# Optimization experiments

Hardware: AMD Instinct MI355X
Metric: run time of the kernel (lower is better)

## Reference

```python
import jax, jax.numpy as jnp
import numpy as np

B, S, D, H, F, E, K = 2, 2048, 1024, 16, 4096, 8, 2
EPS = 1e-6


def setup_inputs() -> dict:
    key = jax.random.key(0)
    ks = jax.random.split(key, 9)
    s = 0.02
    return {
        "x": jax.random.normal(ks[0], (B, S, D), jnp.float32),
        "n1_w": jnp.ones((D,), jnp.float32),
        "n2_w": jnp.ones((D,), jnp.float32),
        "wq": jax.random.normal(ks[1], (D, D), jnp.float32) * s,
        "wk": jax.random.normal(ks[2], (D, D), jnp.float32) * s,
        "wv": jax.random.normal(ks[3], (D, D), jnp.float32) * s,
        "wo": jax.random.normal(ks[4], (D, D), jnp.float32) * s,
        "router_w": jax.random.normal(ks[5], (E, D), jnp.float32) * s,  # nn.Linear(D, E, bias=False)
        "w1": jax.random.normal(ks[6], (E, D, F), jnp.float32) * s,
        "b1": jnp.zeros((E, F), jnp.float32),
        "w2": jax.random.normal(ks[7], (E, F, D), jnp.float32) * s,
        "b2": jnp.zeros((E, D), jnp.float32),
    }


def _rms(t, w):
    return t * w * jax.lax.rsqrt(jnp.mean(t * t, axis=-1, keepdims=True) + EPS)


def reference(x, n1_w, n2_w, wq, wk, wv, wo, router_w, w1, b1, w2, b2):
    hd = D // H
    # --- pre-norm causal multi-head self-attention ---
    h = _rms(x, n1_w)
    q = (h @ wq).reshape(B, S, H, hd)
    k = (h @ wk).reshape(B, S, H, hd)
    v = (h @ wv).reshape(B, S, H, hd)
    scores = jnp.einsum("bqhd,bkhd->bhqk", q, k) * (hd ** -0.5)
    causal = jnp.tril(jnp.ones((S, S), bool))
    scores = jnp.where(causal, scores, jnp.float32(-1e9))
    attn = jax.nn.softmax(scores, axis=-1)
    attn_out = jnp.einsum("bhqk,bkhd->bqhd", attn, v).reshape(B, S, D) @ wo
    x = x + attn_out
    # --- pre-norm MoE MLP: dense experts + top-k weighted combine ---
    h2 = _rms(x, n2_w)
    logits = h2 @ router_w.T                         # [B,S,E]
    probs = jax.nn.softmax(logits, axis=-1)
    topv, topi = jax.lax.top_k(probs, K)             # [B,S,K]
    topv = topv / jnp.sum(topv, axis=-1, keepdims=True)  # renormalized top-k gates
    bi = jnp.arange(B)[:, None, None]
    si = jnp.arange(S)[None, :, None]
    gates = jnp.zeros_like(probs).at[bi, si, topi].set(topv)  # sparse gates [B,S,E]
    eh = jax.nn.gelu(jnp.einsum("bsd,edf->ebsf", h2, w1) + b1[:, None, None, :])
    eo = jnp.einsum("ebsf,efd->ebsd", eh, w2) + b2[:, None, None, :]
    y = jnp.einsum("ebsd,bse->bsd", eo, gates)
    return x + y
```

## Files before the change

kernel.cpp:

```cpp
#include <hip/hip_runtime.h>
#include <hip/hip_bf16.h>


typedef float fx4 __attribute__((ext_vector_type(4)));
typedef short sx4 __attribute__((ext_vector_type(4)));
typedef short sx8 __attribute__((ext_vector_type(8)));
typedef int ix2 __attribute__((ext_vector_type(2)));
typedef int ix4 __attribute__((ext_vector_type(4)));

#define DEVFN static __device__ __forceinline__
#define MFMA16(a, b, c) __builtin_amdgcn_mfma_f32_16x16x32_bf16((a), (b), (c), 0, 0, 0)

typedef __attribute__((address_space(1))) const void GASV;
typedef __attribute__((address_space(3))) void LASV;

DEVFN short f2bf(float f) {
  unsigned u = __float_as_uint(f);
  return (short)((u + 0x7FFFu + ((u >> 16) & 1u)) >> 16);
}
DEVFN float bf2f(short s) { return __uint_as_float(((unsigned)(unsigned short)s) << 16); }

DEVFN int cvt_pk_bf16(float a, float b) {
  int r;
  asm("v_cvt_pk_bf16_f32 %0, %1, %2" : "=v"(r) : "v"(a), "v"(b));
  return r;
}

DEVFN void gll16(const short* g, short* l) {
  __builtin_amdgcn_global_load_lds((GASV*)g, (LASV*)l, 16, 0, 0);
}

template <int BK>
DEVFN int swzr(int row) {
  if constexpr (BK == 64)
    return row & 7;
  else
    return (row ^ (row >> 2)) & 3;
}

DEVFN float fast_gelu(float x) {
  float u = 0.7978845608028654f * (x + 0.044715f * x * x * x);
  float e = __expf(2.0f * u);
  float t = 1.0f - 2.0f / (1.0f + e);
  return 0.5f * x * (1.0f + t);
}

DEVFN float wsum64(float v) {
#pragma unroll
  for (int m = 1; m < 64; m <<= 1) v += __shfl_xor(v, m);
  return v;
}

template <int SPLIT>
__global__ __launch_bounds__(256) void transpose_k(const float* in, short* oh, short* ol,
                                                   int R, int C) {
  __shared__ float t[64][65];
  const int c0 = blockIdx.x * 64, r0 = blockIdx.y * 64;
  const long long bofs = (long long)blockIdx.z * R * C;
  in += bofs;
  oh += bofs;
  if (SPLIT) ol += bofs;
  const int tid = threadIdx.x;
  const int rr = tid >> 4, cc4 = (tid & 15) * 4;
#pragma unroll
  for (int i = 0; i < 4; ++i) {
    int r = i * 16 + rr;
    fx4 v = *(const fx4*)(in + (long long)(r0 + r) * C + c0 + cc4);
    t[r][cc4] = v.x;
    t[r][cc4 + 1] = v.y;
    t[r][cc4 + 2] = v.z;
    t[r][cc4 + 3] = v.w;
  }
  __syncthreads();
#pragma unroll
  for (int i = 0; i < 4; ++i) {
    int oc = i * 16 + rr;
    sx4 hv, lv;
#pragma unroll
    for (int j = 0; j < 4; ++j) {
      float v = t[cc4 + j][oc];
      short hi = f2bf(v);
      hv[j] = hi;
      if (SPLIT) lv[j] = f2bf(v - bf2f(hi));
    }
    *(sx4*)(oh + (long long)(c0 + oc) * R + r0 + cc4) = hv;
    if (SPLIT) *(sx4*)(ol + (long long)(c0 + oc) * R + r0 + cc4) = lv;
  }
}

template <int SPLIT>
__global__ __launch_bounds__(256) void rms_k(const float* x, const float* w, short* hh,
                                             short* hl) {
  const int row = blockIdx.x, tid = threadIdx.x;
  const fx4 v = ((const fx4*)(x + (long long)row * 1024))[tid];
  float ss = v.x * v.x + v.y * v.y + v.z * v.z + v.w * v.w;
  ss = wsum64(ss);
  __shared__ float red[4];
  if ((tid & 63) == 0) red[tid >> 6] = ss;
  __syncthreads();
  ss = red[0] + red[1] + red[2] + red[3];
  const float rr = rsqrtf(ss * (1.0f / 1024.0f) + 1e-6f);
  const fx4 wv = ((const fx4*)w)[tid];
  float vals[4] = {v.x * wv.x * rr, v.y * wv.y * rr, v.z * wv.z * rr, v.w * wv.w * rr};
  sx4 oh, ol;
#pragma unroll
  for (int c = 0; c < 4; ++c) {
    short hi = f2bf(vals[c]);
    oh[c] = hi;
    if (SPLIT) ol[c] = f2bf(vals[c] - bf2f(hi));
  }
  ((sx4*)(hh + (long long)row * 1024))[tid] = oh;
  if (SPLIT) ((sx4*)(hl + (long long)row * 1024))[tid] = ol;
}

struct GemmArgs {
  const short *Ah, *Al, *Bh, *Bl;
  int K, lda, ldb, ldc;
  long long strideBe;
  short *out_h, *out_l;
  float* out_f;
  const float* bias;
  const int* tile_info;
  const float* row_gate;
  const int* row_token;
};

template <int TERMS, int BM, int BK, int BN, int EPI, int PIPE>
__global__ __launch_bounds__(256) void gemm_k(GemmArgs a) {
  const int tid = threadIdx.x, lane = tid & 63, wave = tid >> 6;
  const int gx = gridDim.x;
  const int nwg = gx * (int)gridDim.y;
  int flat = (int)blockIdx.y * gx + (int)blockIdx.x;
  flat = (flat & 7) * (nwg >> 3) + (flat >> 3);
  const int bx = flat % gx;
  const int by = flat / gx;

  int row0, expert = 0, valid = BM;
  if constexpr (EPI == 3 || EPI == 5) {
    const int* ti = a.tile_info + by * 4;
    expert = ti[0];
    row0 = ti[1];
    valid = ti[2];
    if (valid == 0) return;
  } else {
    row0 = by * BM;
  }
  const short* Ap = a.Ah;
  const short* Bp = a.Bh + ((EPI == 3 || EPI == 5) ? (long long)expert * a.strideBe : 0ll);
  const int kbeg = blockIdx.z * a.K;

  constexpr int CH = BK / 8;
  constexpr int NIA = (BM * CH) / 256;
  constexpr int NIB = (BN * CH) / 256;
  constexpr int ASZ = BM * BK;
  constexpr int BSZ = BN * BK;
  constexpr int MI = BM / 32;
  constexpr int TN = BN / 32;
  constexpr int NB = PIPE ? 2 : 1;

  __shared__ short Ash[NB][ASZ];
  __shared__ short Bsh[NB][BSZ];
  __shared__ short Asl[TERMS == 3 ? NB : 1][TERMS == 3 ? ASZ : 1];
  __shared__ short Bsl[TERMS == 3 ? NB : 1][TERMS == 3 ? BSZ : 1];

  fx4 acc[MI][TN] = {};
  const int wr = wave >> 1, wc = wave & 1;

  long long aoff[NIA];
#pragma unroll
  for (int i = 0; i < NIA; ++i) {
    int row = (i * 256 + tid) / CH;
    if constexpr (EPI == 3)
      aoff[i] = (long long)a.row_token[row0 + row] * a.lda;
    else
      aoff[i] = (long long)(row0 + row) * a.lda;
  }

  auto stage = [&](int s, int k0) {
#pragma unroll
    for (int i = 0; i < NIA; ++i) {
      int t = i * 256 + tid;
      int row = t / CH, c = t % CH;
      int cc = c ^ swzr<BK>(row);
      int lbase = (i * 256 + wave * 64) * 8;
      long long acol = kbeg + k0 + cc * 8;
      gll16(Ap + aoff[i] + acol, &Ash[s][lbase]);
      if constexpr (TERMS == 3)
        gll16(a.Al + aoff[i] + acol, &Asl[s][lbase]);
    }
#pragma unroll
    for (int i = 0; i < NIB; ++i) {
      int t = i * 256 + tid;
      int row = t / CH, c = t % CH;
      int cc = c ^ swzr<BK>(row);
      int lbase = (i * 256 + wave * 64) * 8;
      long long acol = kbeg + k0 + cc * 8;
      gll16(Bp + (long long)(bx * BN + row) * a.ldb + acol, &Bsh[s][lbase]);
      if constexpr (TERMS == 3)
        gll16(a.Bl + (long long)(bx * BN + row) * a.ldb + acol, &Bsl[s][lbase]);
    }
  };

  auto compute = [&](int s) {
#pragma unroll
    for (int kk = 0; kk < BK / 32; ++kk) {
      sx8 ah[MI], bh[TN], al_[MI], bl_[TN];
#pragma unroll
      for (int mi = 0; mi < MI; ++mi) {
        int row = wr * (BM / 2) + mi * 16 + (lane & 15);
        int sc = (kk * 4 + (lane >> 4)) ^ swzr<BK>(row);
        ah[mi] = *(const sx8*)&Ash[s][row * BK + sc * 8];
        if constexpr (TERMS == 3) al_[mi] = *(const sx8*)&Asl[s][row * BK + sc * 8];
      }
#pragma unroll
      for (int ni = 0; ni < TN; ++ni) {
        int row = wc * (BN / 2) + ni * 16 + (lane & 15);
        int sc = (kk * 4 + (lane >> 4)) ^ swzr<BK>(row);
        bh[ni] = *(const sx8*)&Bsh[s][row * BK + sc * 8];
        if constexpr (TERMS == 3) bl_[ni] = *(const sx8*)&Bsl[s][row * BK + sc * 8];
      }
#pragma unroll
      for (int mi = 0; mi < MI; ++mi)
#pragma unroll
        for (int ni = 0; ni < TN; ++ni) {
          acc[mi][ni] = MFMA16(ah[mi], bh[ni], acc[mi][ni]);
          if constexpr (TERMS == 3) {
            acc[mi][ni] = MFMA16(ah[mi], bl_[ni], acc[mi][ni]);
            acc[mi][ni] = MFMA16(al_[mi], bh[ni], acc[mi][ni]);
          }
        }
    }
  };

  const int NT = a.K / BK;
  stage(0, 0);
  __syncthreads();
  for (int t = 0; t < NT; ++t) {
    if constexpr (PIPE) {
      if (t + 1 < NT) stage((t + 1) & 1, (t + 1) * BK);
      compute(t & 1);
      if (t + 1 < NT) __syncthreads();
    } else {
      compute(0);
      if (t + 1 < NT) {
        __syncthreads();
        stage(0, (t + 1) * BK);
        __syncthreads();
      }
    }
  }

#pragma unroll
  for (int mi = 0; mi < MI; ++mi)
#pragma unroll
    for (int ni = 0; ni < TN; ++ni) {
      fx4 v = acc[mi][ni];
      int rl = wr * (BM / 2) + mi * 16 + ((lane >> 4) << 2);
      int col = bx * BN + wc * (BN / 2) + ni * 16 + (lane & 15);
#pragma unroll
      for (int j = 0; j < 4; ++j) {
        int r = rl + j;
        long long grow = (long long)row0 + r;
        float xv = v[j];
        if constexpr (EPI == 1) {
          short hi = f2bf(xv);
          a.out_h[grow * a.ldc + col] = hi;
          a.out_l[grow * a.ldc + col] = f2bf(xv - bf2f(hi));
        } else if constexpr (EPI == 3) {
          xv += a.bias[expert * a.ldc + col];
          a.out_h[grow * a.ldc + col] = f2bf(fast_gelu(xv));
        } else if constexpr (EPI == 5) {
          if (r < valid) {
            xv += a.bias[expert * a.ldc + col];
            float g = a.row_gate[grow];
            a.out_h[grow * a.ldc + col] = f2bf(xv * g);
          }
        } else if constexpr (EPI == 6) {
          a.out_f[(long long)blockIdx.z * 4194304 + grow * a.ldc + col] = xv;
        }
      }
    }
}

__global__ __launch_bounds__(256) void combine_wo_k(const float* p0, const float* p1,
                                                    const float* resid, float* out) {
  const long long i = ((long long)blockIdx.x * 256 + threadIdx.x) * 4;
  fx4 a = *(const fx4*)(p0 + i);
  fx4 b = *(const fx4*)(p1 + i);
  fx4 r = *(const fx4*)(resid + i);
  fx4 o;
#pragma unroll
  for (int j = 0; j < 4; ++j) o[j] = a[j] + b[j] + r[j];
  *(fx4*)(out + i) = o;
}

__global__ __launch_bounds__(256) void combine_k(const int* row_of_entry,
                                                 const short* eo, float* out) {
  const int tid = threadIdx.x, lane = tid & 63, wave = tid >> 6;
  const long long token = (long long)blockIdx.x * 4 + wave;
  const int r1 = row_of_entry[token * 2];
  const int r2 = row_of_entry[token * 2 + 1];
  const sx8* e1 = (const sx8*)(eo + (long long)r1 * 1024);
  const sx8* e2 = (const sx8*)(eo + (long long)r2 * 1024);
  float* op = out + token * 1024;
#pragma unroll
  for (int half = 0; half < 2; ++half) {
    sx8 va = e1[lane + half * 64];
    sx8 vb = e2[lane + half * 64];
    int cb = (lane + half * 64) * 8;
#pragma unroll
    for (int q = 0; q < 2; ++q) {
      fx4 o = *(const fx4*)(op + cb + q * 4);
#pragma unroll
      for (int j = 0; j < 4; ++j) o[j] += bf2f(va[q * 4 + j]) + bf2f(vb[q * 4 + j]);
      *(fx4*)(op + cb + q * 4) = o;
    }
  }
}

__global__ __launch_bounds__(128, 2) void flash_k(const short* __restrict__ qkv_h,
                                                  const short* __restrict__ qkv_l,
                                                  short* __restrict__ ao_h,
                                                  short* __restrict__ ao_l) {
  const int tid = threadIdx.x, lane = tid & 63, wave = tid >> 6;
  const int l15 = lane & 15, g = lane >> 4;
  const int qt = (blockIdx.x + blockIdx.y) & 31;
  const int bh = blockIdx.y;
  const int b = bh >> 4, h = bh & 15;
  const long long base = (long long)b * 2048 * 3072;
  const int qw = qt * 64 + wave * 32;

  __shared__ short Kh[4096], Kl[4096];
  __shared__ int VTh[64 * 34], VTl[64 * 34];

  sx8 qh[2][2], ql[2][2];
#pragma unroll
  for (int mb = 0; mb < 2; ++mb)
#pragma unroll
    for (int kk = 0; kk < 2; ++kk) {
      long long qofs =
          base + (long long)(qw + mb * 16 + l15) * 3072 + h * 64 + kk * 32 + g * 8;
      qh[mb][kk] = *(const sx8*)(qkv_h + qofs);
      ql[mb][kk] = *(const sx8*)(qkv_l + qofs);
    }

  fx4 o[2][4] = {};
  float m_r[2] = {-3e38f, -3e38f}, l_r[2] = {0.f, 0.f};

  const int krow0 = tid >> 3;
  const int kc8 = (tid & 7) * 8;
  const int kswz = ((tid & 7) ^ (krow0 & 7)) * 8;
  const int vu = tid >> 3;
  const int vd0 = (tid & 7) * 8;

  sx8 kr[4], krl[4], vr[4], vrl[4];

  auto load_tile = [&](int kt2) {
    const long long tb = base + (long long)(kt2 * 64) * 3072 + h * 64;
#pragma unroll
    for (int s = 0; s < 4; ++s) {
      long long gofs = tb + 1024 + (long long)(s * 16 + krow0) * 3072 + kc8;
      kr[s] = *(const sx8*)(qkv_h + gofs);
      krl[s] = *(const sx8*)(qkv_l + gofs);
    }
#pragma unroll
    for (int k4 = 0; k4 < 4; ++k4) {
      long long gofs = tb + 2048 + (long long)(4 * vu + k4) * 3072 + vd0;
      vr[k4] = *(const sx8*)(qkv_h + gofs);
      vrl[k4] = *(const sx8*)(qkv_l + gofs);
    }
  };

  const int nt = qt + 1;
  load_tile(0);

  for (int kt = 0; kt < nt; ++kt) {
#pragma unroll
    for (int s = 0; s < 4; ++s) {
      *(sx8*)&Kh[(s * 16 + krow0) * 64 + kswz] = kr[s];
      *(sx8*)&Kl[(s * 16 + krow0) * 64 + kswz] = krl[s];
    }
#pragma unroll
    for (int i = 0; i < 8; ++i) {
      int d = vd0 + i;
      ix2 wh, wl;
      wh[0] = (int)(unsigned short)vr[0][i] | ((int)(unsigned short)vr[1][i] << 16);
      wh[1] = (int)(unsigned short)vr[2][i] | ((int)(unsigned short)vr[3][i] << 16);
      wl[0] = (int)(unsigned short)vrl[0][i] | ((int)(unsigned short)vrl[1][i] << 16);
      wl[1] = (int)(unsigned short)vrl[2][i] | ((int)(unsigned short)vrl[3][i] << 16);
      *(ix2*)&VTh[d * 34 + 2 * vu] = wh;
      *(ix2*)&VTl[d * 34 + 2 * vu] = wl;
    }
    __syncthreads();

    if (kt + 1 < nt) load_tile(kt + 1);

    const bool diag = (kt == nt - 1);
    float pvv[2][16];
#pragma unroll
    for (int kc = 0; kc < 4; ++kc) {
      int row = kc * 16 + l15;
      int rsw = row & 7;
      fx4 s0 = {}, s1 = {};
#pragma unroll
      for (int kk = 0; kk < 2; ++kk) {
        int sc = ((kk * 4 + g) ^ rsw) * 8;
        sx8 khf = *(const sx8*)&Kh[row * 64 + sc];
        sx8 klf = *(const sx8*)&Kl[row * 64 + sc];
        s0 = MFMA16(khf, qh[0][kk], s0);
        s1 = MFMA16(khf, qh[1][kk], s1);
        s0 = MFMA16(khf, ql[0][kk], s0);
        s1 = MFMA16(khf, ql[1][kk], s1);
        s0 = MFMA16(klf, qh[0][kk], s0);
        s1 = MFMA16(klf, qh[1][kk], s1);
      }
#pragma unroll
      for (int j = 0; j < 4; ++j) {
        pvv[0][kc * 4 + j] = s0[j];
        pvv[1][kc * 4 + j] = s1[j];
      }
    }

    sx8 pah[2][2], pal[2][2];
#pragma unroll
    for (int mb = 0; mb < 2; ++mb) {
      const int qidx = qw + mb * 16 + l15;
      float t[16];
      float tmax = -3e38f;
#pragma unroll
      for (int i = 0; i < 16; ++i) {
        float sv = pvv[mb][i] * 0.18033688011112f;
        if (diag) {
          int key = kt * 64 + (i >> 2) * 16 + g * 4 + (i & 3);
          sv = (key > qidx) ? -3e38f : sv;
        }
        t[i] = sv;
        tmax = fmaxf(tmax, sv);
      }
      tmax = fmaxf(tmax, __shfl_xor(tmax, 16));
      tmax = fmaxf(tmax, __shfl_xor(tmax, 32));
      if (__any(tmax > m_r[mb] + 8.0f)) {
        float mnew = fmaxf(m_r[mb], tmax);
        float al = exp2f(m_r[mb] - mnew);
        l_r[mb] *= al;
        float aj[4];
#pragma unroll
        for (int j = 0; j < 4; ++j) aj[j] = __shfl(al, (lane & 48) | (g << 2) | j);
#pragma unroll
        for (int f = 0; f < 4; ++f)
#pragma unroll
          for (int j = 0; j < 4; ++j) o[mb][f][j] *= aj[j];
        m_r[mb] = mnew;
      }
      float ps = 0.f;
#pragma unroll
      for (int i = 0; i < 16; ++i) {
        float e = exp2f(t[i] - m_r[mb]);
        t[i] = e;
        ps += e;
      }
      l_r[mb] += ps;
#pragma unroll
      for (int grp = 0; grp < 2; ++grp) {
        ix4 ih, il;
#pragma unroll
        for (int q2 = 0; q2 < 4; ++q2) {
          float a = t[grp * 8 + 2 * q2], bb = t[grp * 8 + 2 * q2 + 1];
          int I = cvt_pk_bf16(a, bb);
          float h0 = __uint_as_float((unsigned)I << 16);
          float h1 = __uint_as_float((unsigned)I & 0xffff0000u);
          int L = cvt_pk_bf16(a - h0, bb - h1);
          ih[q2] = I;
          il[q2] = L;
        }
        pah[mb][grp] = __builtin_bit_cast(sx8, ih);
        pal[mb][grp] = __builtin_bit_cast(sx8, il);
      }
    }

    const ix2* vth = (const ix2*)VTh;
    const ix2* vtl = (const ix2*)VTl;
#pragma unroll
    for (int f = 0; f < 4; ++f) {
      int dd = f * 16 + l15;
      ix2 a0 = vth[dd * 17 + g], a1 = vth[dd * 17 + 4 + g];
      ix2 a2 = vth[dd * 17 + 8 + g], a3 = vth[dd * 17 + 12 + g];
      ix2 c0 = vtl[dd * 17 + g], c1 = vtl[dd * 17 + 4 + g];
      ix2 c2 = vtl[dd * 17 + 8 + g], c3 = vtl[dd * 17 + 12 + g];
      ix4 w;
      w[0] = a0[0]; w[1] = a0[1]; w[2] = a1[0]; w[3] = a1[1];
      sx8 vh8a = __builtin_bit_cast(sx8, w);
      w[0] = a2[0]; w[1] = a2[1]; w[2] = a3[0]; w[3] = a3[1];
      sx8 vh8b = __builtin_bit_cast(sx8, w);
      w[0] = c0[0]; w[1] = c0[1]; w[2] = c1[0]; w[3] = c1[1];
      sx8 vl8a = __builtin_bit_cast(sx8, w);
      w[0] = c2[0]; w[1] = c2[1]; w[2] = c3[0]; w[3] = c3[1];
      sx8 vl8b = __builtin_bit_cast(sx8, w);
#pragma unroll
      for (int mb = 0; mb < 2; ++mb) {
        o[mb][f] = MFMA16(pah[mb][0], vh8a, o[mb][f]);
        o[mb][f] = MFMA16(pah[mb][0], vl8a, o[mb][f]);
        o[mb][f] = MFMA16(pal[mb][0], vh8a, o[mb][f]);
        o[mb][f] = MFMA16(pah[mb][1], vh8b, o[mb][f]);
        o[mb][f] = MFMA16(pah[mb][1], vl8b, o[mb][f]);
        o[mb][f] = MFMA16(pal[mb][1], vh8b, o[mb][f]);
      }
    }
    __syncthreads();
  }

#pragma unroll
  for (int mb = 0; mb < 2; ++mb) {
    float lt = l_r[mb];
    lt += __shfl_xor(lt, 16);
    lt += __shfl_xor(lt, 32);
    float linv = 1.0f / lt;
    float lj[4];
#pragma unroll
    for (int j = 0; j < 4; ++j) lj[j] = __shfl(linv, (lane & 48) | (g << 2) | j);
#pragma unroll
    for (int f = 0; f < 4; ++f)
#pragma unroll
      for (int j = 0; j < 4; ++j) {
        float val = o[mb][f][j] * lj[j];
        long long orow = (long long)b * 2048 + qw + mb * 16 + g * 4 + j;
        int ocol = h * 64 + f * 16 + l15;
        short hi = f2bf(val);
        ao_h[orow * 1024 + ocol] = hi;
        ao_l[orow * 1024 + ocol] = f2bf(val - bf2f(hi));
      }
  }
}

__global__ __launch_bounds__(256) void router_k(const float* x2, const float* w,
                                                const float* rw, int* tok_e,
                                                float* tok_g) {
  const int tid = threadIdx.x, lane = tid & 63, wave = tid >> 6;
  const long long token = (long long)blockIdx.x * 4 + wave;
  const fx4* xr = (const fx4*)(x2 + token * 1024);
  const fx4* wr4 = (const fx4*)w;
  fx4 t[4];
  float ss = 0.0f;
#pragma unroll
  for (int i = 0; i < 4; ++i) {
    fx4 xv = xr[i * 64 + lane];
    fx4 wv = wr4[i * 64 + lane];
    ss += xv.x * xv.x + xv.y * xv.y + xv.z * xv.z + xv.w * xv.w;
    t[i].x = xv.x * wv.x;
    t[i].y = xv.y * wv.y;
    t[i].z = xv.z * wv.z;
    t[i].w = xv.w * wv.w;
  }
  ss = wsum64(ss);
  const float rr = rsqrtf(ss * (1.0f / 1024.0f) + 1e-6f);
  float logit[8];
#pragma unroll
  for (int e = 0; e < 8; ++e) {
    const fx4* re = (const fx4*)(rw + e * 1024);
    float acc = 0.0f;
#pragma unroll
    for (int i = 0; i < 4; ++i) {
      fx4 rv = re[i * 64 + lane];
      acc += t[i].x * rv.x + t[i].y * rv.y + t[i].z * rv.z + t[i].w * rv.w;
    }
    logit[e] = wsum64(acc) * rr;
  }
  float mx = logit[0];
#pragma unroll
  for (int e = 1; e < 8; ++e) mx = fmaxf(mx, logit[e]);
  float pe[8];
#pragma unroll
  for (int e = 0; e < 8; ++e) pe[e] = expf(logit[e] - mx);
  int e1 = 0;
  float b1v = pe[0];
#pragma unroll
  for (int e = 1; e < 8; ++e)
    if (pe[e] > b1v) {
      b1v = pe[e];
      e1 = e;
    }
  int e2 = -1;
  float b2v = -1.0f;
#pragma unroll
  for (int e = 0; e < 8; ++e)
    if (e != e1 && pe[e] > b2v) {
      b2v = pe[e];
      e2 = e;
    }
  if (lane == 0) {
    float inv = 1.0f / (b1v + b2v);
    tok_e[token * 2] = e1;
    tok_e[token * 2 + 1] = e2;
    tok_g[token * 2] = b1v * inv;
    tok_g[token * 2 + 1] = b2v * inv;
  }
}

__global__ __launch_bounds__(1024) void rank_k(const int* tok_e, const float* tok_g,
                                               int* tinfo, int* row_of_entry,
                                               int* row_token, float* row_gate) {
  const int tid = threadIdx.x, lane = tid & 63, wave = tid >> 6;
  __shared__ unsigned wtot[16][4];
  __shared__ unsigned woff[16][4];
  __shared__ int segsh[8];
#pragma unroll
  for (int i = 0; i < 10; ++i) {
    int r = tid * 10 + i;
    if (r < 10240) {
      row_token[r] = 0;
      row_gate[r] = 0.f;
    }
  }
  int e[8];
  {
    const int4* te = (const int4*)tok_e;
    int4 a = te[tid * 2], b = te[tid * 2 + 1];
    e[0] = a.x; e[1] = a.y; e[2] = a.z; e[3] = a.w;
    e[4] = b.x; e[5] = b.y; e[6] = b.z; e[7] = b.w;
  }
  unsigned c0 = 0, c1 = 0, c2 = 0, c3 = 0;
#pragma unroll
  for (int i = 0; i < 8; ++i) {
    unsigned f = 1u << ((e[i] & 1) << 4);
    int h = e[i] >> 1;
    c0 += (h == 0) ? f : 0u;
    c1 += (h == 1) ? f : 0u;
    c2 += (h == 2) ? f : 0u;
    c3 += (h == 3) ? f : 0u;
  }
  unsigned s0 = c0, s1 = c1, s2 = c2, s3 = c3;
#pragma unroll
  for (int d = 1; d < 64; d <<= 1) {
    unsigned t0 = __shfl_up(s0, d), t1 = __shfl_up(s1, d);
    unsigned t2 = __shfl_up(s2, d), t3 = __shfl_up(s3, d);
    if (lane >= d) { s0 += t0; s1 += t1; s2 += t2; s3 += t3; }
  }
  if (lane == 63) {
    wtot[wave][0] = s0; wtot[wave][1] = s1; wtot[wave][2] = s2; wtot[wave][3] = s3;
  }
  __syncthreads();
  if (wave == 0 && lane < 16) {
    unsigned v0 = wtot[lane][0], v1 = wtot[lane][1];
    unsigned v2 = wtot[lane][2], v3 = wtot[lane][3];
    unsigned i0 = v0, i1 = v1, i2 = v2, i3 = v3;
#pragma unroll
    for (int d = 1; d < 16; d <<= 1) {
      unsigned t0 = __shfl_up(i0, d), t1 = __shfl_up(i1, d);
      unsigned t2 = __shfl_up(i2, d), t3 = __shfl_up(i3, d);
      if (lane >= d) { i0 += t0; i1 += t1; i2 += t2; i3 += t3; }
    }
    woff[lane][0] = i0 - v0; woff[lane][1] = i1 - v1;
    woff[lane][2] = i2 - v2; woff[lane][3] = i3 - v3;
    if (lane == 15) {
      wtot[0][0] = i0; wtot[0][1] = i1; wtot[0][2] = i2; wtot[0][3] = i3;
    }
  }
  __syncthreads();
  if (tid == 0) {
    int cnt[8], tte[8], total = 0;
    for (int ee = 0; ee < 8; ++ee) {
      unsigned tot = wtot[0][ee >> 1];
      cnt[ee] = (int)((tot >> ((ee & 1) * 16)) & 0xFFFFu);
      tte[ee] = (cnt[ee] + 63) >> 6;
      total += tte[ee];
    }
    for (int s2 = 0; s2 < 160; ++s2) tinfo[s2 * 4 + 2] = 0;
    int off = 0, i = 0;
    for (int ee = 0; ee < 8; ++ee) {
      segsh[ee] = off;
      for (int t2 = 0; t2 < tte[ee]; ++t2) {
        int slot = (i * 160) / total;
        tinfo[slot * 4 + 0] = ee;
        tinfo[slot * 4 + 1] = off + t2 * 64;
        int v = cnt[ee] - t2 * 64;
        tinfo[slot * 4 + 2] = v > 64 ? 64 : v;
        ++i;
      }
      off += tte[ee] << 6;
    }
  }
  __syncthreads();
  unsigned x0 = woff[wave][0] + s0 - c0;
  unsigned x1 = woff[wave][1] + s1 - c1;
  unsigned x2 = woff[wave][2] + s2 - c2;
  unsigned x3 = woff[wave][3] + s3 - c3;
  const int entry0 = tid * 8;
#pragma unroll
  for (int i = 0; i < 8; ++i) {
    int ee = e[i];
    int h = ee >> 1, sh = (ee & 1) << 4;
    unsigned px = (h == 0) ? x0 : (h == 1) ? x1 : (h == 2) ? x2 : x3;
    int rank = (int)((px >> sh) & 0xFFFFu);
    unsigned f = 1u << sh;
    x0 += (h == 0) ? f : 0u;
    x1 += (h == 1) ? f : 0u;
    x2 += (h == 2) ? f : 0u;
    x3 += (h == 3) ? f : 0u;
    int row = segsh[ee] + rank;
    row_of_entry[entry0 + i] = row;
    row_token[row] = (entry0 + i) >> 1;
    row_gate[row] = tok_g[entry0 + i];
  }
}

extern "C" void kernel_launch(void* const* d_in, const int* in_sizes, int n_in,
                              void* d_out, int out_size, void* d_ws, size_t ws_size,
                              hipStream_t stream) {
  (void)in_sizes;
  (void)n_in;
  (void)out_size;
  (void)ws_size;
  const float* x = (const float*)d_in[0];
  const float* n1w = (const float*)d_in[1];
  const float* n2w = (const float*)d_in[2];
  const float* wq = (const float*)d_in[3];
  const float* wk = (const float*)d_in[4];
  const float* wv = (const float*)d_in[5];
  const float* wo = (const float*)d_in[6];
  const float* rw = (const float*)d_in[7];
  const float* w1 = (const float*)d_in[8];
  const float* b1 = (const float*)d_in[9];
  const float* w2 = (const float*)d_in[10];
  const float* b2 = (const float*)d_in[11];
  float* out = (float*)d_out;
  char* ws = (char*)d_ws;

  short* wqkv_h = (short*)(ws + 0);
  short* wqkv_l = (short*)(ws + 6291456);
  short* wo_h = (short*)(ws + 12582912);
  short* wo_l = (short*)(ws + 14680064);
  short* h_h = (short*)(ws + 16777216);
  short* h_l = (short*)(ws + 25165824);
  short* qkv_h = (short*)(ws + 33554432);
  short* qkv_l = (short*)(ws + 58720256);
  short* ao_h = (short*)(ws + 83886080);
  short* ao_l = (short*)(ws + 92274688);
  float* wo_part = (float*)(ws + 100663296);
  short* h2 = (short*)(ws + 0);
  short* eo = (short*)(ws + 8388608);
  short* wslot = (short*)(ws + 27262976);
  int* row_of_entry = (int*)(ws + 94371840);
  short* eh = (short*)(ws + 100663296);
  char* ctrl = ws + 176160768;
  int* tinfo = (int*)(ctrl + 128);
  int* tok_e = (int*)(ctrl + 4096);
  float* tok_g = (float*)(ctrl + 4096 + 32768);
  int* row_token = (int*)(ctrl + 4096 + 65536);
  float* row_gate = (float*)(ctrl + 4096 + 65536 + 49152);

  transpose_k<1><<<dim3(16, 16, 1), 256, 0, stream>>>(wq, wqkv_h, wqkv_l, 1024, 1024);
  transpose_k<1><<<dim3(16, 16, 1), 256, 0, stream>>>(wk, wqkv_h + 1024 * 1024,
                                                      wqkv_l + 1024 * 1024, 1024, 1024);
  transpose_k<1><<<dim3(16, 16, 1), 256, 0, stream>>>(wv, wqkv_h + 2048 * 1024,
                                                      wqkv_l + 2048 * 1024, 1024, 1024);
  transpose_k<1><<<dim3(16, 16, 1), 256, 0, stream>>>(wo, wo_h, wo_l, 1024, 1024);

  rms_k<1><<<4096, 256, 0, stream>>>(x, n1w, h_h, h_l);

  {
    GemmArgs a = {};
    a.Ah = h_h;
    a.Al = h_l;
    a.Bh = wqkv_h;
    a.Bl = wqkv_l;
    a.K = 1024;
    a.lda = 1024;
    a.ldb = 1024;
    a.ldc = 3072;
    a.out_h = qkv_h;
    a.out_l = qkv_l;
    gemm_k<3, 128, 32, 128, 1, 1><<<dim3(24, 32), 256, 0, stream>>>(a);
  }

  flash_k<<<dim3(32, 32), 128, 0, stream>>>(qkv_h, qkv_l, ao_h, ao_l);

  {
    GemmArgs a = {};
    a.Ah = ao_h;
    a.Al = ao_l;
    a.Bh = wo_h;
    a.Bl = wo_l;
    a.K = 512;
    a.lda = 1024;
    a.ldb = 1024;
    a.ldc = 1024;
    a.out_f = wo_part;
    gemm_k<3, 128, 32, 128, 6, 1><<<dim3(8, 32, 2), 256, 0, stream>>>(a);
  }
  combine_wo_k<<<4096, 256, 0, stream>>>(wo_part, wo_part + 4194304, x, out);

  rms_k<0><<<4096, 256, 0, stream>>>(out, n2w, h2, nullptr);
  router_k<<<1024, 256, 0, stream>>>(out, n2w, rw, tok_e, tok_g);
  rank_k<<<1, 1024, 0, stream>>>(tok_e, tok_g, tinfo, row_of_entry, row_token,
                                 row_gate);

  transpose_k<0><<<dim3(64, 16, 8), 256, 0, stream>>>(w1, wslot, nullptr, 1024, 4096);
  {
    GemmArgs a = {};
    a.Ah = h2;
    a.Bh = wslot;
    a.K = 1024;
    a.lda = 1024;
    a.ldb = 1024;
    a.ldc = 4096;
    a.strideBe = (long long)4096 * 1024;
    a.out_h = eh;
    a.bias = b1;
    a.tile_info = tinfo;
    a.row_token = row_token;
    gemm_k<1, 64, 32, 128, 3, 1><<<dim3(32, 160), 256, 0, stream>>>(a);
  }

  transpose_k<0><<<dim3(16, 64, 8), 256, 0, stream>>>(w2, wslot, nullptr, 4096, 1024);
  {
    GemmArgs a = {};
    a.Ah = eh;
    a.Bh = wslot;
    a.K = 4096;
    a.lda = 4096;
    a.ldb = 4096;
    a.ldc = 1024;
    a.strideBe = (long long)1024 * 4096;
    a.out_h = eo;
    a.bias = b2;
    a.tile_info = tinfo;
    a.row_gate = row_gate;
    gemm_k<1, 64, 32, 64, 5, 1><<<dim3(16, 160), 256, 0, stream>>>(a);
  }

  combine_k<<<1024, 256, 0, stream>>>(row_of_entry, eo, out);
}
```

Before: 717.6 us.

## Fuse residual combine with RMSNorm and double MoE expert tile height

```diff
diff --git a/kernel.cpp b/kernel.cpp
--- a/kernel.cpp
+++ b/kernel.cpp
@@ -282,16 +282,33 @@
     }
 }
 
-__global__ __launch_bounds__(256) void combine_wo_k(const float* p0, const float* p1,
-                                                    const float* resid, float* out) {
-  const long long i = ((long long)blockIdx.x * 256 + threadIdx.x) * 4;
-  fx4 a = *(const fx4*)(p0 + i);
-  fx4 b = *(const fx4*)(p1 + i);
-  fx4 r = *(const fx4*)(resid + i);
+__global__ __launch_bounds__(256) void combine_rms_k(const float* p0, const float* p1,
+                                                     const float* resid, const float* w,
+                                                     float* out, short* h2) {
+  const int row = blockIdx.x, tid = threadIdx.x;
+  const long long base = (long long)row * 1024 + tid * 4;
+  fx4 a = *(const fx4*)(p0 + base);
+  fx4 b = *(const fx4*)(p1 + base);
+  fx4 r = *(const fx4*)(resid + base);
   fx4 o;
-#pragma unroll
-  for (int j = 0; j < 4; ++j) o[j] = a[j] + b[j] + r[j];
-  *(fx4*)(out + i) = o;
+  float ss = 0.f;
+#pragma unroll
+  for (int j = 0; j < 4; ++j) {
+    o[j] = a[j] + b[j] + r[j];
+    ss += o[j] * o[j];
+  }
+  *(fx4*)(out + base) = o;
+  ss = wsum64(ss);
+  __shared__ float red[4];
+  if ((tid & 63) == 0) red[tid >> 6] = ss;
+  __syncthreads();
+  ss = red[0] + red[1] + red[2] + red[3];
+  const float rr = rsqrtf(ss * (1.0f / 1024.0f) + 1e-6f);
+  const fx4 wv = ((const fx4*)w)[tid];
+  sx4 oh;
+#pragma unroll
+  for (int c = 0; c < 4; ++c) oh[c] = f2bf(o[c] * wv[c] * rr);
+  ((sx4*)(h2 + (long long)row * 1024))[tid] = oh;
 }
 
 __global__ __launch_bounds__(256) void combine_k(const int* row_of_entry,
@@ -604,9 +621,9 @@
   __shared__ unsigned woff[16][4];
   __shared__ int segsh[8];
 #pragma unroll
-  for (int i = 0; i < 10; ++i) {
-    int r = tid * 10 + i;
-    if (r < 10240) {
+  for (int i = 0; i < 9; ++i) {
+    int r = tid * 9 + i;
+    if (r < 9216) {
       row_token[r] = 0;
       row_gate[r] = 0.f;
     }
@@ -661,22 +678,22 @@
     for (int ee = 0; ee < 8; ++ee) {
       unsigned tot = wtot[0][ee >> 1];
       cnt[ee] = (int)((tot >> ((ee & 1) * 16)) & 0xFFFFu);
-      tte[ee] = (cnt[ee] + 63) >> 6;
+      tte[ee] = (cnt[ee] + 127) >> 7;
       total += tte[ee];
     }
-    for (int s2 = 0; s2 < 160; ++s2) tinfo[s2 * 4 + 2] = 0;
+    for (int s2 = 0; s2 < 80; ++s2) tinfo[s2 * 4 + 2] = 0;
     int off = 0, i = 0;
     for (int ee = 0; ee < 8; ++ee) {
       segsh[ee] = off;
       for (int t2 = 0; t2 < tte[ee]; ++t2) {
-        int slot = (i * 160) / total;
+        int slot = (i * 80) / total;
         tinfo[slot * 4 + 0] = ee;
-        tinfo[slot * 4 + 1] = off + t2 * 64;
-        int v = cnt[ee] - t2 * 64;
-        tinfo[slot * 4 + 2] = v > 64 ? 64 : v;
+        tinfo[slot * 4 + 1] = off + t2 * 128;
+        int v = cnt[ee] - t2 * 128;
+        tinfo[slot * 4 + 2] = v > 128 ? 128 : v;
         ++i;
       }
-      off += tte[ee] << 6;
+      off += tte[ee] << 7;
     }
   }
   __syncthreads();
@@ -743,10 +760,10 @@
   short* eh = (short*)(ws + 100663296);
   char* ctrl = ws + 176160768;
   int* tinfo = (int*)(ctrl + 128);
-  int* tok_e = (int*)(ctrl + 4096);
-  float* tok_g = (float*)(ctrl + 4096 + 32768);
-  int* row_token = (int*)(ctrl + 4096 + 65536);
-  float* row_gate = (float*)(ctrl + 4096 + 65536 + 49152);
+  int* tok_e = (int*)(ctrl + 2048);
+  float* tok_g = (float*)(ctrl + 2048 + 32768);
+  int* row_token = (int*)(ctrl + 2048 + 65536);
+  float* row_gate = (float*)(ctrl + 2048 + 65536 + 36864);
 
   transpose_k<1><<<dim3(16, 16, 1), 256, 0, stream>>>(wq, wqkv_h, wqkv_l, 1024, 1024);
   transpose_k<1><<<dim3(16, 16, 1), 256, 0, stream>>>(wk, wqkv_h + 1024 * 1024,
@@ -787,9 +804,8 @@
     a.out_f = wo_part;
     gemm_k<3, 128, 32, 128, 6, 1><<<dim3(8, 32, 2), 256, 0, stream>>>(a);
   }
-  combine_wo_k<<<4096, 256, 0, stream>>>(wo_part, wo_part + 4194304, x, out);
-
-  rms_k<0><<<4096, 256, 0, stream>>>(out, n2w, h2, nullptr);
+  combine_rms_k<<<4096, 256, 0, stream>>>(wo_part, wo_part + 4194304, x, n2w, out, h2);
+
   router_k<<<1024, 256, 0, stream>>>(out, n2w, rw, tok_e, tok_g);
   rank_k<<<1, 1024, 0, stream>>>(tok_e, tok_g, tinfo, row_of_entry, row_token,
                                  row_gate);
@@ -808,7 +824,7 @@
     a.bias = b1;
     a.tile_info = tinfo;
     a.row_token = row_token;
-    gemm_k<1, 64, 32, 128, 3, 1><<<dim3(32, 160), 256, 0, stream>>>(a);
+    gemm_k<1, 128, 32, 128, 3, 1><<<dim3(32, 80), 256, 0, stream>>>(a);
   }
 
   transpose_k<0><<<dim3(16, 64, 8), 256, 0, stream>>>(w2, wslot, nullptr, 4096, 1024);
@@ -825,7 +841,7 @@
     a.bias = b2;
     a.tile_info = tinfo;
     a.row_gate = row_gate;
-    gemm_k<1, 64, 32, 64, 5, 1><<<dim3(16, 160), 256, 0, stream>>>(a);
+    gemm_k<1, 128, 64, 64, 5, 1><<<dim3(16, 80), 256, 0, stream>>>(a);
   }
 
   combine_k<<<1024, 256, 0, stream>>>(row_of_entry, eo, out);
```

Result: faster. 653.2 us (-9.0%).
